# Performance work log

Measured on AMD Instinct MI355X. Metric: run time of the kernel, lower is better.

Reference implementation:

```python
import jax, jax.numpy as jnp
import numpy as np

B, S, V, E, H = 64, 512, 32000, 512, 512
EOS_ID = 1  # init kwarg eos_id


def setup_inputs() -> dict:
    key = jax.random.key(0)
    k1, k2, k3, k4 = jax.random.split(key, 4)
    inputs = jax.random.randint(k1, (B, S), 0, V)
    embedding = jax.random.normal(k2, (V, E), jnp.float32) * 0.02
    Wx = jax.random.normal(k3, (E, 4 * H), jnp.float32) * (1.0 / np.sqrt(E))
    Wh = jax.random.normal(k4, (H, 4 * H), jnp.float32) * (1.0 / np.sqrt(H))
    b = jnp.zeros((4 * H,), jnp.float32)
    return {"inputs": inputs, "embedding": embedding, "Wx": Wx, "Wh": Wh, "b": b}


def reference(inputs, embedding, Wx, Wh, b):
    emb = embedding[inputs]            # [B, S, E]
    xs = jnp.swapaxes(emb, 0, 1)       # [S, B, E] -> scan over time
    c0 = jnp.zeros((B, H), emb.dtype)
    h0 = jnp.zeros((B, H), emb.dtype)
    is_eos0 = jnp.zeros((B,), dtype=bool)

    def step(carry, x):
        (c, h), is_eos = carry
        gates = x @ Wx + h @ Wh + b            # [B, 4H]
        i, f, g, o = jnp.split(gates, 4, axis=-1)
        new_c = jax.nn.sigmoid(f) * c + jax.nn.sigmoid(i) * jnp.tanh(g)
        new_h = jax.nn.sigmoid(o) * jnpp_tanh(new_c) if False else jax.nn.sigmoid(o) * jnp.tanh(new_c)
        # EOS-based state freezing: once is_eos is set, carry old state forward
        keep = is_eos[:, None]
        c2 = jnp.where(keep, c, new_c)
        h2 = jnp.where(keep, h, new_h)
        # Faithful to source: EOS flag read from embedded feature at index eos_id
        is_eos = jnp.logical_or(is_eos, x[:, EOS_ID].astype(bool))
        return ((c2, h2), is_eos), new_h

    ((c, h), _), _ = jax.lax.scan(step, ((c0, h0), is_eos0), xs)
    return (c, h)
```

## Files before the change

### kernel.cpp

```cpp
#include <hip/hip_runtime.h>


#define SEQ   512
#define EDIM  512
#define HDIM  512
#define BATCH 64

#define ECHUNKS 8
#define ELEN    (EDIM / ECHUNKS)
#define CTILES  32
#define WS_PARTIAL_OFF 4096

__device__ __forceinline__ float sigf(float x) { return 1.0f / (1.0f + __expf(-x)); }

__global__ __launch_bounds__(512) void gemm_partial_kernel(
    const int* __restrict__ inputs, const float* __restrict__ emb,
    const float* __restrict__ Wx, float* __restrict__ partials)
{
    const int ct = blockIdx.x >> 3;
    const int ec = blockIdx.x & 7;
    const int e0 = ec * ELEN;
    const int t  = threadIdx.x;
    const int lane = t & 63;
    const int w    = __builtin_amdgcn_readfirstlane(t >> 6);
    const int cbase = ct * 64 + w * 8;

    __shared__ float x_s[BATCH][ELEN + 1];

    #pragma unroll
    for (int k = 0; k < 8; ++k) {
        const int b   = w * 8 + k;
        const int tok = inputs[b * SEQ];
        x_s[b][lane] = emb[(size_t)tok * EDIM + e0 + lane];
    }
    __syncthreads();

    float acc[8];
    #pragma unroll
    for (int wc = 0; wc < 8; ++wc) acc[wc] = 0.0f;

    #pragma unroll 4
    for (int e = 0; e < ELEN; ++e) {
        const float xv = x_s[lane][e];
        const float* row = Wx + (size_t)(e0 + e) * 2048 + cbase;
        #pragma unroll
        for (int wc = 0; wc < 8; ++wc)
            acc[wc] += xv * row[wc];
    }

    float* pb = partials + ((size_t)ec * 2048 + cbase) * BATCH + lane;
    #pragma unroll
    for (int wc = 0; wc < 8; ++wc)
        pb[(size_t)wc * BATCH] = acc[wc];
}

__global__ __launch_bounds__(256) void reduce_pointwise_kernel(
    const int* __restrict__ inputs, const float* __restrict__ emb,
    const float* __restrict__ partials, const float* __restrict__ bias,
    float* __restrict__ out, int* __restrict__ eos_flags)
{
    const int g = blockIdx.x * 256 + threadIdx.x;
    const int b = g & 63;
    const int j = g >> 6;

    float gi = bias[j];
    float gg = bias[1024 + j];
    float go = bias[1536 + j];
    #pragma unroll
    for (int ec = 0; ec < ECHUNKS; ++ec) {
        const float* p = partials + (size_t)ec * 2048 * BATCH + b;
        gi += p[(size_t)(j)          * BATCH];
        gg += p[(size_t)(1024 + j)   * BATCH];
        go += p[(size_t)(1536 + j)   * BATCH];
    }

    const float c = sigf(gi) * tanhf(gg);
    const float h = sigf(go) * tanhf(c);
    out[b * HDIM + j]                  = c;
    out[BATCH * HDIM + b * HDIM + j]   = h;

    if (blockIdx.x == 0 && threadIdx.x < BATCH) {
        const int bb  = threadIdx.x;
        const int tok = inputs[bb * SEQ];
        eos_flags[bb] = (emb[(size_t)tok * EDIM + 1] != 0.0f) ? 1 : 0;
    }
}

__global__ __launch_bounds__(512) void tail_kernel(
    const int* __restrict__ inputs, const float* __restrict__ emb,
    const float* __restrict__ Wx, const float* __restrict__ Wh,
    const float* __restrict__ bias, float* __restrict__ out,
    const int* __restrict__ eos_flags)
{
    const int b = blockIdx.x;
    if (eos_flags[b]) return;

    const int t = threadIdx.x;
    __shared__ float h_s[HDIM];
    __shared__ float c_s[HDIM];
    __shared__ float x_s[EDIM];

    c_s[t] = out[b * HDIM + t];
    h_s[t] = out[BATCH * HDIM + b * HDIM + t];
    bool eos = false;
    __syncthreads();

    for (int s = 1; s < SEQ; ++s) {
        const int tok = inputs[b * SEQ + s];
        x_s[t] = emb[(size_t)tok * EDIM + t];
        __syncthreads();

        float g0 = bias[t];
        float g1 = bias[512 + t];
        float g2 = bias[1024 + t];
        float g3 = bias[1536 + t];
        for (int e = 0; e < EDIM; ++e) {
            const float xv = x_s[e];
            const float hv = h_s[e];
            const float* wxr = Wx + (size_t)e * 2048;
            const float* whr = Wh + (size_t)e * 2048;
            g0 += xv * wxr[t]        + hv * whr[t];
            g1 += xv * wxr[512 + t]  + hv * whr[512 + t];
            g2 += xv * wxr[1024 + t] + hv * whr[1024 + t];
            g3 += xv * wxr[1536 + t] + hv * whr[1536 + t];
        }
        const float nc = sigf(g1) * c_s[t] + sigf(g0) * tanhf(g2);
        const float nh = sigf(g3) * tanhf(nc);
        eos = eos || (x_s[1] != 0.0f);
        __syncthreads();
        c_s[t] = nc;
        h_s[t] = nh;
        __syncthreads();
        if (eos) break;
    }

    out[b * HDIM + t]                = c_s[t];
    out[BATCH * HDIM + b * HDIM + t] = h_s[t];
}

extern "C" void kernel_launch(void* const* d_in, const int* in_sizes, int n_in,
                              void* d_out, int out_size, void* d_ws, size_t ws_size,
                              hipStream_t stream) {
    const int*   inputs = (const int*)  d_in[0];
    const float* emb    = (const float*)d_in[1];
    const float* Wx     = (const float*)d_in[2];
    const float* Wh     = (const float*)d_in[3];
    const float* bias   = (const float*)d_in[4];
    float* out   = (float*)d_out;
    int*   flags = (int*)d_ws;
    float* partials = (float*)((char*)d_ws + WS_PARTIAL_OFF);

    gemm_partial_kernel<<<CTILES * ECHUNKS, 512, 0, stream>>>(inputs, emb, Wx, partials);
    reduce_pointwise_kernel<<<(BATCH * HDIM) / 256, 256, 0, stream>>>(
        inputs, emb, partials, bias, out, flags);
    tail_kernel<<<BATCH, 512, 0, stream>>>(inputs, emb, Wx, Wh, bias, out, flags);
}
```

Measured before the change: 15.22 us.

## Fuse reduce/pointwise into tail kernel, skip forget-gate columns, transpose partial layout

Merges the reduce-pointwise and tail kernels into one launch, with one block per batch row that reduces the partials, applies the first-step activations and, for rows not frozen by EOS, continues the recurrence. The first-step GEMM now computes only the i, g and o gate columns (1536 instead of 2048), since c0 is zero and the forget gate has no effect on step one. Partials are staged through shared memory so they are written batch-major and read contiguously. This removes one kernel launch and the flag round trip through global memory, and cuts first-step GEMM work by a quarter. In exchange the reduction now runs on only 64 blocks instead of 128, and the partial writes need an extra shared-memory transpose.

```diff
diff --git a/kernel.cpp b/kernel.cpp
--- a/kernel.cpp
+++ b/kernel.cpp
@@ -1,15 +1,14 @@
 #include <hip/hip_runtime.h>
 
 
-#define SEQ   512
-#define EDIM  512
-#define HDIM  512
-#define BATCH 64
-
-#define ECHUNKS 8
-#define ELEN    (EDIM / ECHUNKS)
-#define CTILES  32
-#define WS_PARTIAL_OFF 4096
+#define SEQ      512
+#define EDIM     512
+#define HDIM     512
+#define BATCH    64
+#define NCOMPACT 1536
+#define ECHUNKS  8
+#define ELEN     (EDIM / ECHUNKS)
+#define CTILES   (NCOMPACT / 64)
 
 __device__ __forceinline__ float sigf(float x) { return 1.0f / (1.0f + __expf(-x)); }
 
@@ -17,125 +16,123 @@
     const int* __restrict__ inputs, const float* __restrict__ emb,
     const float* __restrict__ Wx, float* __restrict__ partials)
 {
-    const int ct = blockIdx.x >> 3;
-    const int ec = blockIdx.x & 7;
-    const int e0 = ec * ELEN;
-    const int t  = threadIdx.x;
+    const int ct   = blockIdx.x >> 3;
+    const int ec   = blockIdx.x & 7;
+    const int e0   = ec * ELEN;
+    const int t    = threadIdx.x;
     const int lane = t & 63;
     const int w    = __builtin_amdgcn_readfirstlane(t >> 6);
-    const int cbase = ct * 64 + w * 8;
+    const int gate = ct >> 3;
+    const int gofs = (gate == 0) ? 0 : (gate == 1 ? 1024 : 1536);
+    const int wcol = gofs + (ct & 7) * 64 + w * 8;
 
-    __shared__ float x_s[BATCH][ELEN + 1];
+    __shared__ float x_s[ELEN][BATCH + 1];
+    __shared__ float g_s[64][BATCH + 1];
 
     #pragma unroll
     for (int k = 0; k < 8; ++k) {
         const int b   = w * 8 + k;
         const int tok = inputs[b * SEQ];
-        x_s[b][lane] = emb[(size_t)tok * EDIM + e0 + lane];
+        x_s[lane][b] = emb[(size_t)tok * EDIM + e0 + lane];
     }
     __syncthreads();
 
-    float acc[8];
-    #pragma unroll
-    for (int wc = 0; wc < 8; ++wc) acc[wc] = 0.0f;
-
-    #pragma unroll 4
+    float acc[8] = {};
+    #pragma unroll 8
     for (int e = 0; e < ELEN; ++e) {
-        const float xv = x_s[lane][e];
-        const float* row = Wx + (size_t)(e0 + e) * 2048 + cbase;
+        const float xv = x_s[e][lane];
+        const float* row = Wx + (size_t)(e0 + e) * 2048 + wcol;
         #pragma unroll
         for (int wc = 0; wc < 8; ++wc)
             acc[wc] += xv * row[wc];
     }
 
-    float* pb = partials + ((size_t)ec * 2048 + cbase) * BATCH + lane;
     #pragma unroll
     for (int wc = 0; wc < 8; ++wc)
-        pb[(size_t)wc * BATCH] = acc[wc];
+        g_s[w * 8 + wc][lane] = acc[wc];
+    __syncthreads();
+
+    #pragma unroll
+    for (int k = 0; k < 8; ++k) {
+        const int b = w * 8 + k;
+        partials[((size_t)ec * BATCH + b) * NCOMPACT + ct * 64 + lane] = g_s[lane][b];
+    }
 }
 
-__global__ __launch_bounds__(256) void reduce_pointwise_kernel(
+__global__ __launch_bounds__(512) void reduce_pointwise_tail_kernel(
     const int* __restrict__ inputs, const float* __restrict__ emb,
-    const float* __restrict__ partials, const float* __restrict__ bias,
-    float* __restrict__ out, int* __restrict__ eos_flags)
+    const float* __restrict__ Wx, const float* __restrict__ Wh,
+    const float* __restrict__ bias, const float* __restrict__ partials,
+    float* __restrict__ out)
 {
-    const int g = blockIdx.x * 256 + threadIdx.x;
-    const int b = g & 63;
-    const int j = g >> 6;
+    const int b = blockIdx.x;
+    const int j = threadIdx.x;
+
+    __shared__ float h_s[HDIM];
+    __shared__ float c_s[HDIM];
+    __shared__ float x_s[EDIM];
 
     float gi = bias[j];
     float gg = bias[1024 + j];
     float go = bias[1536 + j];
     #pragma unroll
     for (int ec = 0; ec < ECHUNKS; ++ec) {
-        const float* p = partials + (size_t)ec * 2048 * BATCH + b;
-        gi += p[(size_t)(j)          * BATCH];
-        gg += p[(size_t)(1024 + j)   * BATCH];
-        go += p[(size_t)(1536 + j)   * BATCH];
+        const float* p = partials + ((size_t)ec * BATCH + b) * NCOMPACT;
+        gi += p[j];
+        gg += p[512 + j];
+        go += p[1024 + j];
     }
 
-    const float c = sigf(gi) * tanhf(gg);
-    const float h = sigf(go) * tanhf(c);
-    out[b * HDIM + j]                  = c;
-    out[BATCH * HDIM + b * HDIM + j]   = h;
+    float c = sigf(gi) * tanhf(gg);
+    float h = sigf(go) * tanhf(c);
 
-    if (blockIdx.x == 0 && threadIdx.x < BATCH) {
-        const int bb  = threadIdx.x;
-        const int tok = inputs[bb * SEQ];
-        eos_flags[bb] = (emb[(size_t)tok * EDIM + 1] != 0.0f) ? 1 : 0;
+    const int tok0 = inputs[b * SEQ];
+    const bool frozen = (emb[(size_t)tok0 * EDIM + 1] != 0.0f);
+
+    if (frozen) {
+        out[b * HDIM + j]                = c;
+        out[BATCH * HDIM + b * HDIM + j] = h;
+        return;
     }
-}
 
-__global__ __launch_bounds__(512) void tail_kernel(
-    const int* __restrict__ inputs, const float* __restrict__ emb,
-    const float* __restrict__ Wx, const float* __restrict__ Wh,
-    const float* __restrict__ bias, float* __restrict__ out,
-    const int* __restrict__ eos_flags)
-{
-    const int b = blockIdx.x;
-    if (eos_flags[b]) return;
-
-    const int t = threadIdx.x;
-    __shared__ float h_s[HDIM];
-    __shared__ float c_s[HDIM];
-    __shared__ float x_s[EDIM];
-
-    c_s[t] = out[b * HDIM + t];
-    h_s[t] = out[BATCH * HDIM + b * HDIM + t];
+    c_s[j] = c;
+    h_s[j] = h;
     bool eos = false;
     __syncthreads();
 
+    const float b0 = bias[j];
+    const float b1 = bias[512 + j];
+    const float b2 = bias[1024 + j];
+    const float b3 = bias[1536 + j];
+
     for (int s = 1; s < SEQ; ++s) {
         const int tok = inputs[b * SEQ + s];
-        x_s[t] = emb[(size_t)tok * EDIM + t];
+        x_s[j] = emb[(size_t)tok * EDIM + j];
         __syncthreads();
 
-        float g0 = bias[t];
-        float g1 = bias[512 + t];
-        float g2 = bias[1024 + t];
-        float g3 = bias[1536 + t];
+        float g0 = b0, g1 = b1, g2 = b2, g3 = b3;
         for (int e = 0; e < EDIM; ++e) {
             const float xv = x_s[e];
             const float hv = h_s[e];
             const float* wxr = Wx + (size_t)e * 2048;
             const float* whr = Wh + (size_t)e * 2048;
-            g0 += xv * wxr[t]        + hv * whr[t];
-            g1 += xv * wxr[512 + t]  + hv * whr[512 + t];
-            g2 += xv * wxr[1024 + t] + hv * whr[1024 + t];
-            g3 += xv * wxr[1536 + t] + hv * whr[1536 + t];
+            g0 += xv * wxr[j]        + hv * whr[j];
+            g1 += xv * wxr[512 + j]  + hv * whr[512 + j];
+            g2 += xv * wxr[1024 + j] + hv * whr[1024 + j];
+            g3 += xv * wxr[1536 + j] + hv * whr[1536 + j];
         }
-        const float nc = sigf(g1) * c_s[t] + sigf(g0) * tanhf(g2);
+        const float nc = sigf(g1) * c_s[j] + sigf(g0) * tanhf(g2);
         const float nh = sigf(g3) * tanhf(nc);
         eos = eos || (x_s[1] != 0.0f);
         __syncthreads();
-        c_s[t] = nc;
-        h_s[t] = nh;
+        c_s[j] = nc;
+        h_s[j] = nh;
         __syncthreads();
         if (eos) break;
     }
 
-    out[b * HDIM + t]                = c_s[t];
-    out[BATCH * HDIM + b * HDIM + t] = h_s[t];
+    out[b * HDIM + j]                = c_s[j];
+    out[BATCH * HDIM + b * HDIM + j] = h_s[j];
 }
 
 extern "C" void kernel_launch(void* const* d_in, const int* in_sizes, int n_in,
@@ -146,12 +143,10 @@
     const float* Wx     = (const float*)d_in[2];
     const float* Wh     = (const float*)d_in[3];
     const float* bias   = (const float*)d_in[4];
-    float* out   = (float*)d_out;
-    int*   flags = (int*)d_ws;
-    float* partials = (float*)((char*)d_ws + WS_PARTIAL_OFF);
+    float* out      = (float*)d_out;
+    float* partials = (float*)d_ws;
 
     gemm_partial_kernel<<<CTILES * ECHUNKS, 512, 0, stream>>>(inputs, emb, Wx, partials);
-    reduce_pointwise_kernel<<<(BATCH * HDIM) / 256, 256, 0, stream>>>(
-        inputs, emb, partials, bias, out, flags);
-    tail_kernel<<<BATCH, 512, 0, stream>>>(inputs, emb, Wx, Wh, bias, out, flags);
+    reduce_pointwise_tail_kernel<<<BATCH, 512, 0, stream>>>(
+        inputs, emb, Wx, Wh, bias, partials, out);
 }
```

New measurement: 13.14 us, median of 2. 13.7% less time.
